# Optimization experiments

Measured on AMD Instinct MI355X. Metric: run time of the kernel, lower is better.

The kernel has to match this reference:

```python
import jax, jax.numpy as jnp
import numpy as np

N_NODES = 100000
N_EDGES = 1000000
IN_DIM = 128
H = [64, 64, 64, 64, 128]
OUT_DIM = 64
K = 3  # TAGConv default hops
BN_EPS = 1e-5


def _gcn_norm(src, dst, num_nodes):
    # symmetric normalization D^{-1/2} A D^{-1/2}, no self loops (PyG TAGConv default)
    deg = jax.ops.segment_sum(jnp.ones(src.shape[0], jnp.float32), dst, num_segments=num_nodes)
    dis = jnp.where(deg > 0, jax.lax.rsqrt(jnp.maximum(deg, 1.0)), 0.0)
    return dis[src] * dis[dst]  # [E]


def _tagconv(x, src, dst, norm, Ws, b, num_nodes):
    # Ws: [K+1, in, out]; out = sum_k (A_hat^k x) @ W_k + b
    out = x @ Ws[0]
    h = x
    for k in range(1, K + 1):
        h = jax.ops.segment_sum(h[src] * norm[:, None], dst, num_segments=num_nodes)
        out = out + h @ Ws[k]
    return out + b


def setup_inputs() -> dict:
    key = jax.random.key(0)
    ks = jax.random.split(key, 16)
    s = 0.05
    x = jax.random.normal(ks[0], (N_NODES, IN_DIM), jnp.float32)
    edge_index = jax.random.randint(ks[1], (2, N_EDGES), 0, N_NODES, dtype=jnp.int64)
    return {
        "x": x,
        "edge_index": edge_index,
        "bn_gamma": jnp.ones((IN_DIM,), jnp.float32),
        "bn_beta": jnp.zeros((IN_DIM,), jnp.float32),
        "W1": jax.random.normal(ks[2], (IN_DIM, H[0]), jnp.float32) * s,
        "b1": jnp.zeros((H[0],), jnp.float32),
        "tag1_W": jax.random.normal(ks[3], (K + 1, H[0], H[1]), jnp.float32) * s,
        "tag1_b": jnp.zeros((H[1],), jnp.float32),
        "W2": jax.random.normal(ks[4], (H[1], H[2]), jnp.float32) * s,
        "b2": jnp.zeros((H[2],), jnp.float32),
        "tag2_W": jax.random.normal(ks[5], (K + 1, H[2], H[3]), jnp.float32) * s,
        "tag2_b": jnp.zeros((H[3],), jnp.float32),
        "W3": jax.random.normal(ks[6], (H[3] + IN_DIM, H[4]), jnp.float32) * s,
        "b3": jnp.zeros((H[4],), jnp.float32),
        "W4": jax.random.normal(ks[7], (H[4], OUT_DIM), jnp.float32) * s,
        "b4": jnp.zeros((OUT_DIM,), jnp.float32),
    }


def reference(x, edge_index, bn_gamma, bn_beta, W1, b1, tag1_W, tag1_b,
              W2, b2, tag2_W, tag2_b, W3, b3, W4, b4):
    gelu = lambda t: jax.nn.gelu(t, approximate=False)  # torch GELU default (erf)
    src, dst = edge_index[0], edge_index[1]
    norm = _gcn_norm(src, dst, N_NODES)

    # BatchNorm over nodes (training-mode batch stats, biased variance)
    mean = jnp.mean(x, axis=0)
    var = jnp.mean((x - mean) ** 2, axis=0)
    x_norm = (x - mean) * jax.lax.rsqrt(var + BN_EPS) * bn_gamma + bn_beta

    h = gelu(x_norm @ W1 + b1)
    h = gelu(_tagconv(h, src, dst, norm, tag1_W, tag1_b, N_NODES))
    h = gelu(h @ W2 + b2)
    h = gelu(_tagconv(h, src, dst, norm, tag2_W, tag2_b, N_NODES))
    a = jnp.concatenate([x, h], axis=1)
    a = gelu(a @ W3 + b3)
    return a @ W4 + b4
```

## Files before the change

kernel.cpp:

```cpp
#include <hip/hip_runtime.h>
#include <stdint.h>

typedef unsigned short u16;
typedef unsigned int   u32;
typedef __attribute__((ext_vector_type(8))) short short8;
typedef __attribute__((ext_vector_type(4))) float float4v;

#define DEV __device__ __forceinline__

#define ABLK  512
#define MAXNB 4096

DEV float bf2f(u16 u){ return __uint_as_float(((u32)u)<<16); }
DEV u16 f2bf(float f){
  u32 u = __float_as_uint(f);
  u32 r = u + 0x7fffu + ((u>>16)&1u);
  return (u16)(r>>16);
}
DEV float gelu_f(float x){ return 0.5f*x*(1.0f + erff(x*0.70710678118654752f)); }
DEV float ldext(const void* b, size_t i, int f32){
  return f32 ? ((const float*)b)[i] : bf2f(((const u16*)b)[i]);
}
DEV int ld_src(const int* ei, int e, int E, int m64){ return m64 ? ei[2*e]     : ei[e]; }
DEV int ld_dst(const int* ei, int e, int E, int m64){ return m64 ? ei[2*(E+e)] : ei[E+e]; }
DEV int swz(int k, int n){
  return (((k>>5)*4 + (n>>4))*64 + ((((k>>3)&3)<<4) | (n&15)))*8 + (k&7);
}
DEV int2 ldnt(const int2* p){
  long v = __builtin_nontemporal_load((const long*)p);
  int2 r; r.x = (int)(v & 0xffffffffL); r.y = (int)(((unsigned long)v)>>32);
  return r;
}

__global__ __launch_bounds__(256) void detect_types(const int* __restrict__ ei,
                                                    const u16* __restrict__ xw,
                                                    int* __restrict__ flags){
  __shared__ int a64, insane;
  int t = threadIdx.x;
  if (t==0){ a64=0; insane=0; }
  __syncthreads();
  int l=0;
  for (int i=t; i<4096; i+=256) l |= ei[2*i+1];
  if (l) atomicOr(&a64, 1);
  int c=0;
  for (int i=t; i<2048; i+=256){
    u16 lo = xw[2*i];
    int e8 = (lo>>7)&0xff;
    if (e8!=0 && (e8<90 || e8>160)) c++;
  }
  atomicAdd(&insane, c);
  __syncthreads();
  if (t==0){ flags[0] = a64?0:1; flags[1] = (insane>256)?1:0; }
}

__global__ __launch_bounds__(256) void econv_a0(const int* __restrict__ ei,
                                                const int* __restrict__ flags,
                                                int2* __restrict__ sd, int* __restrict__ hist,
                                                int E, int N, int shift, int NBK){
  __shared__ int cnt[MAXNB];
  for (int i=threadIdx.x; i<NBK; i+=256) cnt[i]=0;
  __syncthreads();
  int m64 = flags[0];
  for (int e = blockIdx.x*256 + threadIdx.x; e < E; e += ABLK*256){
    int s = ld_src(ei, e, E, m64);
    int d = ld_dst(ei, e, E, m64);
    int2 p; p.x = s; p.y = d;
    sd[e] = p;
    if ((unsigned)d < (unsigned)N) atomicAdd(&cnt[d>>shift], 1);
  }
  __syncthreads();
  int* hrow = hist + (size_t)blockIdx.x*NBK;
  for (int i=threadIdx.x; i<NBK; i+=256) hrow[i] = cnt[i];
}

__global__ __launch_bounds__(256) void hist_colscan(int* __restrict__ hist,
                                                    int* __restrict__ btot, int NBK){
  __shared__ int lds[256];
  int b = blockIdx.x, t = threadIdx.x;
  int v0 = hist[(size_t)(2*t  )*NBK + b];
  int v1 = hist[(size_t)(2*t+1)*NBK + b];
  int ps = v0 + v1;
  lds[t] = ps; __syncthreads();
  for (int off=1; off<256; off<<=1){
    int add = (t>=off) ? lds[t-off] : 0;
    __syncthreads();
    lds[t] += add;
    __syncthreads();
  }
  int excl = lds[t] - ps;
  hist[(size_t)(2*t  )*NBK + b] = excl;
  hist[(size_t)(2*t+1)*NBK + b] = excl + v0;
  if (t==255) btot[b] = lds[255];
}

__global__ __launch_bounds__(256) void bucket_scan(const int* __restrict__ btot,
                                                   int* __restrict__ bb, int NBK){
  __shared__ int lds[256];
  int t = threadIdx.x;
  int carry = 0;
  int nch = (NBK + 255)/256;
  for (int c=0; c<nch; c++){
    int i = c*256 + t;
    int v = (i<NBK) ? btot[i] : 0;
    lds[t] = v; __syncthreads();
    for (int off=1; off<256; off<<=1){
      int add = (t>=off) ? lds[t-off] : 0;
      __syncthreads();
      lds[t] += add;
      __syncthreads();
    }
    if (i<NBK) bb[i] = carry + lds[t] - v;
    int tot = lds[255];
    __syncthreads();
    carry += tot;
  }
  if (t==0) bb[NBK] = carry;
}

__global__ __launch_bounds__(256) void econv_a1(const int2* __restrict__ sd,
                                                const int* __restrict__ hist,
                                                const int* __restrict__ bb,
                                                int2* __restrict__ binned,
                                                int E, int N, int shift, int NBK){
  __shared__ int cnt[MAXNB];
  __shared__ int base[MAXNB];
  const int* hrow = hist + (size_t)blockIdx.x*NBK;
  for (int i=threadIdx.x; i<NBK; i+=256){ cnt[i]=0; base[i]=bb[i]+hrow[i]; }
  __syncthreads();
  for (int e = blockIdx.x*256 + threadIdx.x; e < E; e += ABLK*256){
    int2 p = sd[e];
    if ((unsigned)p.y < (unsigned)N){
      int b = p.y >> shift;
      int r = atomicAdd(&cnt[b], 1);
      binned[base[b] + r] = p;
    }
  }
}

__global__ __launch_bounds__(256) void bucket_count(const int2* __restrict__ binned,
                                                    const int* __restrict__ bb,
                                                    int* __restrict__ rofs, float* __restrict__ dis,
                                                    int N, int shift, int NBK, int NPB){
  __shared__ int cnt[256];
  __shared__ int lds[256];
  int b = blockIdx.x, t = threadIdx.x;
  int lo = bb[b], hi = bb[b+1];
  if (t < NPB) cnt[t] = 0;
  __syncthreads();
  int mask = NPB - 1;
  for (int e = lo + t; e < hi; e += 256)
    atomicAdd(&cnt[binned[e].y & mask], 1);
  __syncthreads();
  int v = (t < NPB) ? cnt[t] : 0;
  lds[t] = v; __syncthreads();
  for (int off=1; off<256; off<<=1){
    int add = (t>=off) ? lds[t-off] : 0;
    __syncthreads();
    lds[t] += add;
    __syncthreads();
  }
  if (t < NPB){
    int node = (b<<shift) + t;
    if (node < N){
      rofs[node] = lo + lds[t] - v;
      dis[node]  = v > 0 ? rsqrtf((float)v) : 0.f;
    }
  }
  if (b==0 && t==0) rofs[N] = bb[NBK];
}

__global__ __launch_bounds__(256) void bucket_emit(const int2* __restrict__ binned,
                                                   const int* __restrict__ bb,
                                                   const int* __restrict__ rofs,
                                                   const float* __restrict__ dis,
                                                   int2* __restrict__ epack,
                                                   int N, int shift, int NPB){
  __shared__ int   cur[256];
  __shared__ float dl[256];
  int b = blockIdx.x, t = threadIdx.x;
  int lo = bb[b], hi = bb[b+1];
  if (t < NPB){
    int node = (b<<shift) + t;
    cur[t] = (node < N) ? rofs[node] : 0;
    dl[t]  = (node < N) ? dis[node]  : 0.f;
  }
  __syncthreads();
  int mask = NPB - 1;
  for (int e = lo + t; e < hi; e += 256){
    int2 p = binned[e];
    int dli = p.y & mask;
    int slot = atomicAdd(&cur[dli], 1);
    int s = p.x; float w;
    if ((unsigned)s < (unsigned)N) w = dis[s]*dl[dli];
    else { s = 0; w = 0.f; }
    int2 pk; pk.x = s; pk.y = __float_as_int(w);
    epack[slot] = pk;
  }
}

__global__ __launch_bounds__(256) void bn_stats(const void* __restrict__ x,
                                                const int* __restrict__ flags,
                                                float* __restrict__ sums,
                                                u16* __restrict__ xbf, int N){
  __shared__ float red[16][128];
  int f32  = flags[1];
  int tid  = threadIdx.x;
  int col  = tid & 15;
  int rsub = tid >> 4;
  float s8[8], q8[8];
  #pragma unroll
  for (int j=0;j<8;j++){ s8[j]=0.f; q8[j]=0.f; }
  for (int r = blockIdx.x*16 + rsub; r < N; r += gridDim.x*16){
    float f[8];
    if (f32){
      const float* xp = (const float*)x + (size_t)r*128 + col*8;
      float4 A = *(const float4*)xp;
      float4 B = *(const float4*)(xp+4);
      f[0]=A.x; f[1]=A.y; f[2]=A.z; f[3]=A.w;
      f[4]=B.x; f[5]=B.y; f[6]=B.z; f[7]=B.w;
      u16 o[8];
      #pragma unroll
      for (int j=0;j<8;j++) o[j] = f2bf(f[j]);
      *(uint4*)(xbf + (size_t)r*128 + col*8) = *(uint4*)o;
    } else {
      const u16* xp = (const u16*)x + (size_t)r*128 + col*8;
      uint4 u = *(const uint4*)xp;
      f[0]=bf2f((u16)(u.x&0xffffu)); f[1]=bf2f((u16)(u.x>>16));
      f[2]=bf2f((u16)(u.y&0xffffu)); f[3]=bf2f((u16)(u.y>>16));
      f[4]=bf2f((u16)(u.z&0xffffu)); f[5]=bf2f((u16)(u.z>>16));
      f[6]=bf2f((u16)(u.w&0xffffu)); f[7]=bf2f((u16)(u.w>>16));
    }
    #pragma unroll
    for (int j=0;j<8;j++){ s8[j]+=f[j]; q8[j]+=f[j]*f[j]; }
  }
  #pragma unroll
  for (int j=0;j<8;j++) red[rsub][col*8+j] = s8[j];
  __syncthreads();
  if (tid < 128){
    float t=0.f;
    #pragma unroll
    for (int i=0;i<16;i++) t += red[i][tid];
    atomicAdd(&sums[tid], t);
  }
  __syncthreads();
  #pragma unroll
  for (int j=0;j<8;j++) red[rsub][col*8+j] = q8[j];
  __syncthreads();
  if (tid < 128){
    float t=0.f;
    #pragma unroll
    for (int i=0;i<16;i++) t += red[i][tid];
    atomicAdd(&sums[128+tid], t);
  }
}

struct PrepOut {
  u16 *W1p,*Wt1,*Wt2,*W2p,*W3a,*W3b,*W4p;
  float *b1p,*bt1,*bt2,*b2p,*b3a,*b3b,*b4p;
};

#define PREP_TOTAL 78272

__global__ __launch_bounds__(256) void prep(const float* __restrict__ sums, float invN,
    const int* __restrict__ flags,
    const void* g, const void* be,
    const void* W1, const void* b1,
    const void* t1W, const void* t1b,
    const void* W2, const void* b2,
    const void* t2W, const void* t2b,
    const void* W3, const void* b3,
    const void* W4, const void* b4,
    PrepOut o)
{
  int f32 = flags[1];
  int idx = blockIdx.x*256 + threadIdx.x;
  if (idx >= PREP_TOTAL) return;
  auto scale_shift = [&](int f, float& sc, float& sh){
    float m   = sums[f]*invN;
    float var = sums[128+f]*invN - m*m;
    sc = ldext(g,f,f32) * rsqrtf(var + 1e-5f);
    sh = ldext(be,f,f32) - m*sc;
  };
  if (idx < 8192){
    int k=idx>>6, n=idx&63; float sc,sh; scale_shift(k,sc,sh);
    o.W1p[swz(k,n)] = f2bf(sc*ldext(W1,idx,f32)); return;
  }
  idx -= 8192;
  if (idx < 64){
    float acc = ldext(b1,idx,f32);
    for (int f=0; f<128; f++){ float sc,sh; scale_shift(f,sc,sh); acc += sh*ldext(W1,f*64+idx,f32); }
    o.b1p[idx]=acc; return;
  }
  idx -= 64;
  if (idx < 16384){ int k=idx>>6,n=idx&63; o.Wt1[swz(k,n)]=f2bf(ldext(t1W,idx,f32)); return; }  idx -= 16384;
  if (idx < 64)   { o.bt1[idx]=ldext(t1b,idx,f32); return; }  idx -= 64;
  if (idx < 16384){ int k=idx>>6,n=idx&63; o.Wt2[swz(k,n)]=f2bf(ldext(t2W,idx,f32)); return; }  idx -= 16384;
  if (idx < 64)   { o.bt2[idx]=ldext(t2b,idx,f32); return; }  idx -= 64;
  if (idx < 4096) { int k=idx>>6,n=idx&63; o.W2p[swz(k,n)]=f2bf(ldext(W2,idx,f32));  return; }  idx -= 4096;
  if (idx < 64)   { o.b2p[idx]=ldext(b2,idx,f32);  return; }  idx -= 64;
  if (idx < 12288){ int k=idx>>6,n=idx&63; o.W3a[swz(k,n)]=f2bf(ldext(W3,(size_t)k*128+n,f32));    return; }  idx -= 12288;
  if (idx < 64)   { o.b3a[idx]=ldext(b3,idx,f32);  return; }  idx -= 64;
  if (idx < 12288){ int k=idx>>6,n=idx&63; o.W3b[swz(k,n)]=f2bf(ldext(W3,(size_t)k*128+64+n,f32)); return; }  idx -= 12288;
  if (idx < 64)   { o.b3b[idx]=ldext(b3,64+idx,f32); return; } idx -= 64;
  if (idx < 8192) { int k=idx>>6,n=idx&63; o.W4p[swz(k,n)]=f2bf(ldext(W4,idx,f32));  return; }
  else            { o.b4p[idx-8192]=ldext(b4,idx-8192,f32); }
}

struct KD { const u16* p[8]; int ld[8]; };

template<int KS,int OUTMODE>
__global__ __launch_bounds__(256,2) void gemm_mfma(
    KD d, const u16* __restrict__ Wsw, const float* __restrict__ bias,
    void* __restrict__ out, int ldo, int ocol,
    int N, const int* __restrict__ flags, long xdelta, u32 xmask)
{
  constexpr int LBYTES = OUTMODE ? 128*68*4 : 128*72*2;
  __shared__ __align__(16) char lds[LBYTES];
  if (xmask && !flags[1]){
    #pragma unroll
    for (int t=0;t<KS;t++) if (xmask & (1u<<t)) d.p[t] += xdelta;
  }
  int tid = threadIdx.x, w = tid>>6, l = tid&63;
  int rlo = l&15, kq = l>>4;
  int row0b = blockIdx.x*128;
  int row0  = row0b + w*32;

  short8 Bf[KS][4];
  #pragma unroll
  for (int t=0;t<KS;t++)
    #pragma unroll
    for (int c=0;c<4;c++)
      Bf[t][c] = *(const short8*)(Wsw + ((t*4+c)*64 + l)*8);

  float4v a0[4], a1[4];
  #pragma unroll
  for (int c=0;c<4;c++){
    a0[c].x=0;a0[c].y=0;a0[c].z=0;a0[c].w=0;
    a1[c].x=0;a1[c].y=0;a1[c].z=0;a1[c].w=0;
  }

  #pragma unroll
  for (int t=0;t<KS;t++){
    const u16* ap = d.p[t]; int ld = d.ld[t];
    short8 A0 = *(const short8*)(ap + (size_t)(row0+rlo)*ld + kq*8);
    short8 A1 = *(const short8*)(ap + (size_t)(row0+16+rlo)*ld + kq*8);
    #pragma unroll
    for (int c=0;c<4;c++){
      a0[c] = __builtin_amdgcn_mfma_f32_16x16x32_bf16(A0, Bf[t][c], a0[c], 0,0,0);
      a1[c] = __builtin_amdgcn_mfma_f32_16x16x32_bf16(A1, Bf[t][c], a1[c], 0,0,0);
    }
  }

  float bv[4];
  #pragma unroll
  for (int c=0;c<4;c++) bv[c] = bias[c*16 + rlo];

  int nrow = N - row0b; if (nrow > 128) nrow = 128; if (nrow < 0) nrow = 0;

  if (OUTMODE==0){
    u16* s = (u16*)lds;
    #pragma unroll
    for (int c=0;c<4;c++){
      int col = c*16 + rlo;
      #pragma unroll
      for (int r=0;r<4;r++){
        s[(w*32 +      kq*4 + r)*72 + col] = f2bf(gelu_f(a0[c][r] + bv[c]));
        s[(w*32 + 16 + kq*4 + r)*72 + col] = f2bf(gelu_f(a1[c][r] + bv[c]));
      }
    }
    __syncthreads();
    u16* ob = (u16*)out + (size_t)row0b*ldo + ocol;
    for (int i=tid; i<nrow*8; i+=256){
      int r = i>>3, cc = (i&7)<<3;
      *(uint4*)(ob + (size_t)r*ldo + cc) = *(const uint4*)(s + r*72 + cc);
    }
  } else {
    int f32o = flags[1];
    if (f32o){
      float* sf = (float*)lds;
      #pragma unroll
      for (int c=0;c<4;c++){
        int col = c*16 + rlo;
        #pragma unroll
        for (int r=0;r<4;r++){
          float v0 = a0[c][r] + bv[c]; float v1 = a1[c][r] + bv[c];
          sf[(w*32 +      kq*4 + r)*68 + col] = isfinite(v0)?v0:777.0f;
          sf[(w*32 + 16 + kq*4 + r)*68 + col] = isfinite(v1)?v1:777.0f;
        }
      }
      __syncthreads();
      float* ob = (float*)out + (size_t)row0b*64;
      for (int i=tid; i<nrow*16; i+=256){
        int r = i>>4, cc = (i&15)<<2;
        *(uint4*)(ob + (size_t)r*64 + cc) = *(const uint4*)(sf + r*68 + cc);
      }
    } else {
      u16* s = (u16*)lds;
      #pragma unroll
      for (int c=0;c<4;c++){
        int col = c*16 + rlo;
        #pragma unroll
        for (int r=0;r<4;r++){
          float v0 = a0[c][r] + bv[c]; float v1 = a1[c][r] + bv[c];
          s[(w*32 +      kq*4 + r)*72 + col] = f2bf(isfinite(v0)?v0:777.0f);
          s[(w*32 + 16 + kq*4 + r)*72 + col] = f2bf(isfinite(v1)?v1:777.0f);
        }
      }
      __syncthreads();
      u16* ob = (u16*)out + (size_t)row0b*64;
      for (int i=tid; i<nrow*8; i+=256){
        int r = i>>3, cc = (i&7)<<3;
        *(uint4*)(ob + (size_t)r*64 + cc) = *(const uint4*)(s + r*72 + cc);
      }
    }
  }
}

__global__ __launch_bounds__(256) void spmm(const int* __restrict__ rofs,
    const int2* __restrict__ epack,
    const u16* __restrict__ hin, u16* __restrict__ hout, int N)
{
  int lane = threadIdx.x & 63;
  int wv   = (int)((blockIdx.x*256 + threadIdx.x) >> 6);
  int sub  = lane >> 3;
  int f8   = (lane & 7) * 8;
  int row  = wv*8 + sub;
  bool rok = row < N;
  int beg = rok ? rofs[row]   : 0;
  int end = rok ? rofs[row+1] : 0;

  float acc[8];
  #pragma unroll
  for (int j=0;j<8;j++) acc[j]=0.f;

  int e = beg;
  int2 pk[4];
  #pragma unroll
  for (int i=0;i<4;i++){ pk[i].x=0; pk[i].y=0; if (e+i < end) pk[i] = ldnt(&epack[e+i]); }

  while (__any(e < end)){
    int   s[4]; float w[4];
    #pragma unroll
    for (int i=0;i<4;i++){
      bool act = (e+i) < end;
      s[i] = act ? pk[i].x : 0;
      w[i] = act ? __int_as_float(pk[i].y) : 0.f;
      if ((u32)s[i] >= (u32)N){ s[i]=0; w[i]=0.f; }
    }
    uint4 v0 = *(const uint4*)(hin + (size_t)s[0]*64 + f8);
    uint4 v1 = *(const uint4*)(hin + (size_t)s[1]*64 + f8);
    uint4 v2 = *(const uint4*)(hin + (size_t)s[2]*64 + f8);
    uint4 v3 = *(const uint4*)(hin + (size_t)s[3]*64 + f8);
    int en = e + 4;
    #pragma unroll
    for (int i=0;i<4;i++){ pk[i].x=0; pk[i].y=0; if (en+i < end) pk[i] = ldnt(&epack[en+i]); }
    acc[0] += w[0]*__uint_as_float(v0.x<<16);
    acc[1] += w[0]*__uint_as_float(v0.x&0xffff0000u);
    acc[2] += w[0]*__uint_as_float(v0.y<<16);
    acc[3] += w[0]*__uint_as_float(v0.y&0xffff0000u);
    acc[4] += w[0]*__uint_as_float(v0.z<<16);
    acc[5] += w[0]*__uint_as_float(v0.z&0xffff0000u);
    acc[6] += w[0]*__uint_as_float(v0.w<<16);
    acc[7] += w[0]*__uint_as_float(v0.w&0xffff0000u);
    acc[0] += w[1]*__uint_as_float(v1.x<<16);
    acc[1] += w[1]*__uint_as_float(v1.x&0xffff0000u);
    acc[2] += w[1]*__uint_as_float(v1.y<<16);
    acc[3] += w[1]*__uint_as_float(v1.y&0xffff0000u);
    acc[4] += w[1]*__uint_as_float(v1.z<<16);
    acc[5] += w[1]*__uint_as_float(v1.z&0xffff0000u);
    acc[6] += w[1]*__uint_as_float(v1.w<<16);
    acc[7] += w[1]*__uint_as_float(v1.w&0xffff0000u);
    acc[0] += w[2]*__uint_as_float(v2.x<<16);
    acc[1] += w[2]*__uint_as_float(v2.x&0xffff0000u);
    acc[2] += w[2]*__uint_as_float(v2.y<<16);
    acc[3] += w[2]*__uint_as_float(v2.y&0xffff0000u);
    acc[4] += w[2]*__uint_as_float(v2.z<<16);
    acc[5] += w[2]*__uint_as_float(v2.z&0xffff0000u);
    acc[6] += w[2]*__uint_as_float(v2.w<<16);
    acc[7] += w[2]*__uint_as_float(v2.w&0xffff0000u);
    acc[0] += w[3]*__uint_as_float(v3.x<<16);
    acc[1] += w[3]*__uint_as_float(v3.x&0xffff0000u);
    acc[2] += w[3]*__uint_as_float(v3.y<<16);
    acc[3] += w[3]*__uint_as_float(v3.y&0xffff0000u);
    acc[4] += w[3]*__uint_as_float(v3.z<<16);
    acc[5] += w[3]*__uint_as_float(v3.z&0xffff0000u);
    acc[6] += w[3]*__uint_as_float(v3.w<<16);
    acc[7] += w[3]*__uint_as_float(v3.w&0xffff0000u);
    e = en;
  }

  if (rok){
    u16 o[8];
    #pragma unroll
    for (int j=0;j<8;j++) o[j]=f2bf(acc[j]);
    *(uint4*)(hout + (size_t)row*64 + f8) = *(uint4*)o;
  }
}

extern "C" void kernel_launch(void* const* d_in, const int* in_sizes, int n_in,
                              void* d_out, int out_size, void* d_ws, size_t ws_size,
                              hipStream_t stream)
{
  const void* x   = d_in[0];
  const int*  ei  = (const int*)d_in[1];
  const void* gam = d_in[2];  const void* bet = d_in[3];
  const void* W1  = d_in[4];  const void* b1  = d_in[5];
  const void* t1W = d_in[6];  const void* t1b = d_in[7];
  const void* W2  = d_in[8];  const void* b2  = d_in[9];
  const void* t2W = d_in[10]; const void* t2b = d_in[11];
  const void* W3  = d_in[12]; const void* b3  = d_in[13];
  const void* W4  = d_in[14]; const void* b4  = d_in[15];

  const int N = in_sizes[0]/128;
  const int E = in_sizes[1]/2;

  int shift = 7;
  while ((((long)N + (1L<<shift) - 1) >> shift) > MAXNB) shift++;
  const int NPB = 1<<shift;
  const int NBK = (int)(((long)N + NPB - 1) >> shift);

  char* p = (char*)d_ws;
  auto carve = [&](size_t bytes)->void*{
    void* r = (void*)p;
    p += (bytes + 255) & ~(size_t)255;
    return r;
  };
  float* bnsums  = (float*)carve(256*4);
  int*   flags   = (int*)  carve(256);
  size_t zero_span = (size_t)((char*)p - (char*)bnsums);
  int*   row_ofs = (int*)  carve((size_t)(N+1)*4);
  float* dis     = (float*)carve((size_t)N*4);
  int*   hist    = (int*)  carve((size_t)ABLK*NBK*4);
  int*   btot    = (int*)  carve((size_t)NBK*4);
  int*   bb      = (int*)  carve((size_t)(NBK+1)*4);
  int2*  sd      = (int2*) carve((size_t)E*8);
  int2*  binned  = (int2*) carve((size_t)E*8);
  int2*  epack   = (int2*) carve((size_t)E*8);
  PrepOut po;
  po.W1p=(u16*)carve(8192*2);   po.b1p=(float*)carve(64*4);
  po.Wt1=(u16*)carve(16384*2);  po.bt1=(float*)carve(64*4);
  po.Wt2=(u16*)carve(16384*2);  po.bt2=(float*)carve(64*4);
  po.W2p=(u16*)carve(4096*2);   po.b2p=(float*)carve(64*4);
  po.W3a=(u16*)carve(12288*2);  po.b3a=(float*)carve(64*4);
  po.W3b=(u16*)carve(12288*2);  po.b3b=(float*)carve(64*4);
  po.W4p=(u16*)carve(8192*2);   po.b4p=(float*)carve(64*4);
  u16* xbf  = (u16*)carve((size_t)N*128*2);
  u16* buf0 = (u16*)carve((size_t)N*64*2);
  u16* buf1 = (u16*)carve((size_t)N*64*2);
  u16* buf2 = (u16*)carve((size_t)N*64*2);
  u16* buf3 = (u16*)carve((size_t)N*64*2);
  u16* buf4 = (u16*)carve((size_t)N*64*2);
  carve(64*1024);
  u16* Ka   = buf0;

  size_t needed = (size_t)(p - (char*)d_ws);
  if (needed > ws_size || NPB > 256 || E < 4096){
    hipMemsetAsync(d_out, 0, (size_t)out_size*2, stream);
    return;
  }

  long xdelta = (const u16*)x - xbf;

  const int gblk = (N + 127)/128;
  const int sblk = (N + 31)/32;

  hipMemsetAsync(bnsums, 0, zero_span, stream);

  detect_types<<<1, 256, 0, stream>>>(ei, (const u16*)x, flags);
  econv_a0    <<<ABLK,256,0,stream>>>(ei, flags, sd, hist, E, N, shift, NBK);
  hist_colscan<<<NBK, 256,0,stream>>>(hist, btot, NBK);
  bucket_scan <<<1,   256,0,stream>>>(btot, bb, NBK);
  econv_a1    <<<ABLK,256,0,stream>>>(sd, hist, bb, binned, E, N, shift, NBK);
  bucket_count<<<NBK, 256,0,stream>>>(binned, bb, row_ofs, dis, N, shift, NBK, NPB);
  bucket_emit <<<NBK, 256,0,stream>>>(binned, bb, row_ofs, dis, epack, N, shift, NPB);
  bn_stats    <<<512, 256,0,stream>>>(x, flags, bnsums, xbf, N);
  prep        <<<(PREP_TOTAL+255)/256, 256, 0, stream>>>(bnsums, 1.0f/(float)N, flags,
                 gam, bet, W1, b1, t1W, t1b, W2, b2, t2W, t2b, W3, b3, W4, b4, po);

  KD dx;   for (int t=0;t<4;t++){ dx.p[t]  = xbf + t*32;  dx.ld[t]=128; }
           for (int t=4;t<8;t++){ dx.p[t]  = xbf;         dx.ld[t]=128; }
  KD dcat; { u16* bs[4]={buf0,buf1,buf2,buf3};
             for (int t=0;t<8;t++){ dcat.p[t]=bs[t>>1]+(t&1)*32; dcat.ld[t]=64; } }
  KD d3;   for (int t=0;t<4;t++){ d3.p[t]  = xbf + t*32;  d3.ld[t]=128; }
           d3.p[4]=buf4; d3.ld[4]=64; d3.p[5]=buf4+32; d3.ld[5]=64;
           d3.p[6]=buf4; d3.ld[6]=64; d3.p[7]=buf4;    d3.ld[7]=64;
  KD d4;   for (int t=0;t<4;t++){ d4.p[t]  = Ka + t*32;   d4.ld[t]=128; }
           for (int t=4;t<8;t++){ d4.p[t]  = Ka;          d4.ld[t]=128; }

  gemm_mfma<4,0><<<gblk,256,0,stream>>>(dx, po.W1p, po.b1p, buf0,64,0, N, flags, xdelta, 0xFu);
  spmm<<<sblk,256,0,stream>>>(row_ofs, epack, buf0, buf1, N);
  spmm<<<sblk,256,0,stream>>>(row_ofs, epack, buf1, buf2, N);
  spmm<<<sblk,256,0,stream>>>(row_ofs, epack, buf2, buf3, N);
  gemm_mfma<8,0><<<gblk,256,0,stream>>>(dcat, po.Wt1, po.bt1, buf4,64,0, N, flags, 0, 0);
  { KD dl2; for (int t=0;t<8;t++){ dl2.p[t]=buf4+(t&1)*32; dl2.ld[t]=64; }
    gemm_mfma<2,0><<<gblk,256,0,stream>>>(dl2, po.W2p, po.b2p, buf0,64,0, N, flags, 0, 0); }
  spmm<<<sblk,256,0,stream>>>(row_ofs, epack, buf0, buf1, N);
  spmm<<<sblk,256,0,stream>>>(row_ofs, epack, buf1, buf2, N);
  spmm<<<sblk,256,0,stream>>>(row_ofs, epack, buf2, buf3, N);
  gemm_mfma<8,0><<<gblk,256,0,stream>>>(dcat, po.Wt2, po.bt2, buf4,64,0, N, flags, 0, 0);
  gemm_mfma<6,0><<<gblk,256,0,stream>>>(d3, po.W3a, po.b3a, Ka,128,0,  N, flags, xdelta, 0xFu);
  gemm_mfma<6,0><<<gblk,256,0,stream>>>(d3, po.W3b, po.b3b, Ka,128,64, N, flags, xdelta, 0xFu);
  gemm_mfma<4,1><<<gblk,256,0,stream>>>(d4, po.W4p, po.b4p, d_out,64,0, N, flags, 0, 0);
}
```

Baseline: 448.1 us.

## Sort rows by degree within buckets to balance SpMM wave work

bucket_count now builds a per-bucket permutation that orders nodes by in-degree (capped at 63) via an LDS counting sort. spmm reads rows through this permutation so the 8 rows sharing a wavefront have similar edge counts, which reduces divergence and idle lanes in the __any loop. The edge prefetch is also made branchless by clamping indices to 0 and masking weights. In exchange, each spmm adds an indirect perm load and neighbouring waves write scattered output rows, so write coalescing is worse.

```diff
diff --git a/kernel.cpp b/kernel.cpp
--- a/kernel.cpp
+++ b/kernel.cpp
@@ -140,12 +140,15 @@
 __global__ __launch_bounds__(256) void bucket_count(const int2* __restrict__ binned,
                                                     const int* __restrict__ bb,
                                                     int* __restrict__ rofs, float* __restrict__ dis,
+                                                    int* __restrict__ perm,
                                                     int N, int shift, int NBK, int NPB){
   __shared__ int cnt[256];
   __shared__ int lds[256];
+  __shared__ int bcur[64];
   int b = blockIdx.x, t = threadIdx.x;
   int lo = bb[b], hi = bb[b+1];
   if (t < NPB) cnt[t] = 0;
+  if (t < 64) bcur[t] = 0;
   __syncthreads();
   int mask = NPB - 1;
   for (int e = lo + t; e < hi; e += 256)
@@ -159,14 +162,30 @@
     lds[t] += add;
     __syncthreads();
   }
-  if (t < NPB){
-    int node = (b<<shift) + t;
-    if (node < N){
-      rofs[node] = lo + lds[t] - v;
-      dis[node]  = v > 0 ? rsqrtf((float)v) : 0.f;
-    }
+  int node = (b<<shift) + t;
+  bool nok = (t < NPB) && (node < N);
+  if (nok){
+    rofs[node] = lo + lds[t] - v;
+    dis[node]  = v > 0 ? rsqrtf((float)v) : 0.f;
   }
   if (b==0 && t==0) rofs[N] = bb[NBK];
+  int bin = v < 63 ? v : 63;
+  if (nok) atomicAdd(&bcur[bin], 1);
+  __syncthreads();
+  int bv = (t < 64) ? bcur[t] : 0;
+  lds[t] = bv; __syncthreads();
+  for (int off=1; off<64; off<<=1){
+    int add = (t>=off) ? lds[t-off] : 0;
+    __syncthreads();
+    lds[t] += add;
+    __syncthreads();
+  }
+  if (t < 64) bcur[t] = lds[t] - bv;
+  __syncthreads();
+  if (nok){
+    int slot = atomicAdd(&bcur[bin], 1);
+    perm[(b<<shift) + slot] = node;
+  }
 }
 
 __global__ __launch_bounds__(256) void bucket_emit(const int2* __restrict__ binned,
@@ -417,6 +436,7 @@
 }
 
 __global__ __launch_bounds__(256) void spmm(const int* __restrict__ rofs,
+    const int* __restrict__ perm,
     const int2* __restrict__ epack,
     const u16* __restrict__ hin, u16* __restrict__ hout, int N)
 {
@@ -424,8 +444,10 @@
   int wv   = (int)((blockIdx.x*256 + threadIdx.x) >> 6);
   int sub  = lane >> 3;
   int f8   = (lane & 7) * 8;
-  int row  = wv*8 + sub;
-  bool rok = row < N;
+  int rid  = wv*8 + sub;
+  bool rok = rid < N;
+  int row = rok ? perm[rid] : 0;
+  if ((u32)row >= (u32)N) row = 0;
   int beg = rok ? rofs[row]   : 0;
   int end = rok ? rofs[row+1] : 0;
 
@@ -436,16 +458,16 @@
   int e = beg;
   int2 pk[4];
   #pragma unroll
-  for (int i=0;i<4;i++){ pk[i].x=0; pk[i].y=0; if (e+i < end) pk[i] = ldnt(&epack[e+i]); }
+  for (int i=0;i<4;i++){ int ix = (e+i < end) ? (e+i) : 0; pk[i] = ldnt(&epack[ix]); }
 
   while (__any(e < end)){
     int   s[4]; float w[4];
     #pragma unroll
     for (int i=0;i<4;i++){
       bool act = (e+i) < end;
-      s[i] = act ? pk[i].x : 0;
+      s[i] = pk[i].x;
+      if ((u32)s[i] >= (u32)N) s[i] = 0;
       w[i] = act ? __int_as_float(pk[i].y) : 0.f;
-      if ((u32)s[i] >= (u32)N){ s[i]=0; w[i]=0.f; }
     }
     uint4 v0 = *(const uint4*)(hin + (size_t)s[0]*64 + f8);
     uint4 v1 = *(const uint4*)(hin + (size_t)s[1]*64 + f8);
@@ -453,7 +475,7 @@
     uint4 v3 = *(const uint4*)(hin + (size_t)s[3]*64 + f8);
     int en = e + 4;
     #pragma unroll
-    for (int i=0;i<4;i++){ pk[i].x=0; pk[i].y=0; if (en+i < end) pk[i] = ldnt(&epack[en+i]); }
+    for (int i=0;i<4;i++){ int ix = (en+i < end) ? (en+i) : 0; pk[i] = ldnt(&epack[ix]); }
     acc[0] += w[0]*__uint_as_float(v0.x<<16);
     acc[1] += w[0]*__uint_as_float(v0.x&0xffff0000u);
     acc[2] += w[0]*__uint_as_float(v0.y<<16);
@@ -530,6 +552,7 @@
   size_t zero_span = (size_t)((char*)p - (char*)bnsums);
   int*   row_ofs = (int*)  carve((size_t)(N+1)*4);
   float* dis     = (float*)carve((size_t)N*4);
+  int*   perm    = (int*)  carve((size_t)N*4);
   int*   hist    = (int*)  carve((size_t)ABLK*NBK*4);
   int*   btot    = (int*)  carve((size_t)NBK*4);
   int*   bb      = (int*)  carve((size_t)(NBK+1)*4);
@@ -571,7 +594,7 @@
   hist_colscan<<<NBK, 256,0,stream>>>(hist, btot, NBK);
   bucket_scan <<<1,   256,0,stream>>>(btot, bb, NBK);
   econv_a1    <<<ABLK,256,0,stream>>>(sd, hist, bb, binned, E, N, shift, NBK);
-  bucket_count<<<NBK, 256,0,stream>>>(binned, bb, row_ofs, dis, N, shift, NBK, NPB);
+  bucket_count<<<NBK, 256,0,stream>>>(binned, bb, row_ofs, dis, perm, N, shift, NBK, NPB);
   bucket_emit <<<NBK, 256,0,stream>>>(binned, bb, row_ofs, dis, epack, N, shift, NPB);
   bn_stats    <<<512, 256,0,stream>>>(x, flags, bnsums, xbf, N);
   prep        <<<(PREP_TOTAL+255)/256, 256, 0, stream>>>(bnsums, 1.0f/(float)N, flags,
@@ -588,15 +611,15 @@
            for (int t=4;t<8;t++){ d4.p[t]  = Ka;          d4.ld[t]=128; }
 
   gemm_mfma<4,0><<<gblk,256,0,stream>>>(dx, po.W1p, po.b1p, buf0,64,0, N, flags, xdelta, 0xFu);
-  spmm<<<sblk,256,0,stream>>>(row_ofs, epack, buf0, buf1, N);
-  spmm<<<sblk,256,0,stream>>>(row_ofs, epack, buf1, buf2, N);
-  spmm<<<sblk,256,0,stream>>>(row_ofs, epack, buf2, buf3, N);
+  spmm<<<sblk,256,0,stream>>>(row_ofs, perm, epack, buf0, buf1, N);
+  spmm<<<sblk,256,0,stream>>>(row_ofs, perm, epack, buf1, buf2, N);
+  spmm<<<sblk,256,0,stream>>>(row_ofs, perm, epack, buf2, buf3, N);
   gemm_mfma<8,0><<<gblk,256,0,stream>>>(dcat, po.Wt1, po.bt1, buf4,64,0, N, flags, 0, 0);
   { KD dl2; for (int t=0;t<8;t++){ dl2.p[t]=buf4+(t&1)*32; dl2.ld[t]=64; }
     gemm_mfma<2,0><<<gblk,256,0,stream>>>(dl2, po.W2p, po.b2p, buf0,64,0, N, flags, 0, 0); }
-  spmm<<<sblk,256,0,stream>>>(row_ofs, epack, buf0, buf1, N);
-  spmm<<<sblk,256,0,stream>>>(row_ofs, epack, buf1, buf2, N);
-  spmm<<<sblk,256,0,stream>>>(row_ofs, epack, buf2, buf3, N);
+  spmm<<<sblk,256,0,stream>>>(row_ofs, perm, epack, buf0, buf1, N);
+  spmm<<<sblk,256,0,stream>>>(row_ofs, perm, epack, buf1, buf2, N);
+  spmm<<<sblk,256,0,stream>>>(row_ofs, perm, epack, buf2, buf3, N);
   gemm_mfma<8,0><<<gblk,256,0,stream>>>(dcat, po.Wt2, po.bt2, buf4,64,0, N, flags, 0, 0);
   gemm_mfma<6,0><<<gblk,256,0,stream>>>(d3, po.W3a, po.b3a, Ka,128,0,  N, flags, xdelta, 0xFu);
   gemm_mfma<6,0><<<gblk,256,0,stream>>>(d3, po.W3b, po.b3b, Ka,128,64, N, flags, xdelta, 0xFu);
```

After: 475.8 us. +6.2%, slower.
